# Optimization experiments

Measured on AMD Instinct MI355X. Metric: run time of the kernel, lower is better.

The kernel has to match this reference:

```python
import jax, jax.numpy as jnp
import numpy as np

B, T, E = 4, 2048, 512      # batch, seq_len, embedding_dim
H, D = 8, 64                # n_heads, head_size


def setup_inputs() -> dict:
    key = jax.random.key(0)
    ks = jax.random.split(key, 8)
    rn = lambda k, sh, sc=1.0: jax.random.normal(k, sh, dtype=jnp.float32) * sc
    return {
        "x": rn(ks[0], (B, T, E)),
        "k": rn(ks[1], (B, T, E)),
        "q": rn(ks[2], (B, T, E)),
        "v": rn(ks[3], (B, T, E)),
        # per-head Q/K/V projection weights, stacked: [H, D, E] (bias=False as in nanoGPT-style heads)
        "Wq": rn(ks[4], (H, D, E), E ** -0.5),
        "Wk": rn(ks[5], (H, D, E), E ** -0.5),
        "Wv": rn(ks[6], (H, D, E), E ** -0.5),
        # output projection Linear(H*D -> E)
        "Wo": rn(ks[7], (E, H * D), (H * D) ** -0.5),
        "bo": jnp.zeros((E,), jnp.float32),
    }


def reference(x, k, q, v, Wq, Wk, Wv, Wo, bo):
    # batched equivalent of the per-head Python loop: one einsum per Q/K/V
    qh = jnp.einsum('bte,hde->bhtd', q, Wq)   # [B,H,T,D]
    kh = jnp.einsum('bse,hde->bhsd', k, Wk)
    vh = jnp.einsum('bse,hde->bhsd', v, Wv)
    scores = jnp.einsum('bhtd,bhsd->bhts', qh, kh) * (D ** -0.5)
    Tq = x.shape[1]
    causal = jnp.tril(jnp.ones((Tq, Tq), dtype=bool))  # masked=True: tril mask
    scores = jnp.where(causal, scores, -jnp.inf)
    wei = jax.nn.softmax(scores, axis=-1)              # dropout=0.0 -> identity
    out = jnp.einsum('bhts,bhsd->bhtd', wei, vh)       # [B,H,T,D]
    out = out.transpose(0, 2, 1, 3).reshape(x.shape[0], Tq, H * D)  # concat heads
    return out @ Wo.T + bo                              # final projection
```

## Files before the change

### kernel.cpp

```cpp
#include <hip/hip_runtime.h>
#include <hip/hip_bf16.h>
#include <cstdint>
#include <cstddef>

#define Bb 4
#define Tt 2048
#define Ee 512
#define Hh 8
#define Dd 64
#define HD 512
#define BT 8192

typedef __bf16 bf16x8 __attribute__((ext_vector_type(8)));
typedef __bf16 bf16x4 __attribute__((ext_vector_type(4)));
typedef short s16x4 __attribute__((ext_vector_type(4)));
typedef float f32x4 __attribute__((ext_vector_type(4)));

__device__ __forceinline__ f32x4 mfma16(bf16x8 a, bf16x8 b, f32x4 c) {
  return __builtin_amdgcn_mfma_f32_16x16x32_bf16(a, b, c, 0, 0, 0);
}

__device__ __forceinline__ s16x4 as_s16x4(bf16x4 v) {
  union { bf16x4 b; s16x4 s; } u; u.b = v; return u.s;
}

__device__ __forceinline__ f32x4 mfma16k16(bf16x4 a, bf16x4 b, f32x4 c) {
#if defined(__HIP_DEVICE_COMPILE__)
  return __builtin_amdgcn_mfma_f32_16x16x16bf16_1k(as_s16x4(a), as_s16x4(b), c, 0, 0, 0);
#else
  (void)a; (void)b;
  return c;
#endif
}

typedef __attribute__((address_space(3))) uint32_t lds_u32_t;
typedef const __attribute__((address_space(1))) uint32_t glb_u32_t;
__device__ __forceinline__ void gload16(const void* g, void* l) {
  __builtin_amdgcn_global_load_lds((glb_u32_t*)g, (lds_u32_t*)l, 16, 0, 0);
}

__global__ void cvt_w_kernel(const float* __restrict__ wq, const float* __restrict__ wk,
                             const float* __restrict__ wv, const float* __restrict__ wo,
                             __bf16* __restrict__ dst) {
  int id = blockIdx.x * 256 + threadIdx.x;
  int r = id & 127;
  int lgg = (id >> 7) & 3;
  int p = (id >> 9) & 15;
  int cb = (id >> 13) & 3;
  int m = id >> 15;
  const float* src = (m == 0) ? wq : (m == 1) ? wk : (m == 2) ? wv : wo;
  const float* s = src + (size_t)(cb * 128 + r) * 512 + p * 32 + lgg * 8;
  float4 f0 = *(const float4*)s;
  float4 f1 = *(const float4*)(s + 4);
  bf16x8 o;
  o[0] = (__bf16)f0.x; o[1] = (__bf16)f0.y; o[2] = (__bf16)f0.z; o[3] = (__bf16)f0.w;
  o[4] = (__bf16)f1.x; o[5] = (__bf16)f1.y; o[6] = (__bf16)f1.z; o[7] = (__bf16)f1.w;
  *(bf16x8*)(dst + (size_t)m * 262144 + cb * 65536 + p * 4096 + lgg * 1024 + r * 8) = o;
}

__global__ __launch_bounds__(256)
void gemm_qkv_kernel(const float* __restrict__ Aq, const float* __restrict__ Ak,
                     const float* __restrict__ Av, const __bf16* __restrict__ Wall,
                     __bf16* __restrict__ qh, __bf16* __restrict__ kh, __bf16* __restrict__ vt) {
  const int id = blockIdx.x;
  const int xcd = id & 7, s = id >> 3;
  const int bx = s & 3;
  const int pair = xcd + 8 * (s >> 2);
  const int by = pair & 63;
  const int pz = pair >> 6;

  const float* A = (pz == 0) ? Aq : (pz == 1) ? Ak : Av;
  const char* Bw = (const char*)(Wall + (size_t)pz * 262144 + (size_t)bx * 65536);
  const int row0 = by * 128;
  const int col0 = bx * 128;

  __shared__ __align__(16) __bf16 As[128 * 32];
  __shared__ __align__(16) __bf16 Bs[128 * 32];
  char* As8 = (char*)As;
  char* Bs8 = (char*)Bs;

  const int tid = threadIdx.x;
  const int l = tid & 63, w = tid >> 6;
  const int ln = l & 15, lg = l >> 4;
  const int wr = (w >> 1) * 64, wc = (w & 1) * 64;

  const int sr = tid >> 1;
  const int sce = (tid & 1) * 16;
  const int sbyte = sr * 64 + sce * 2;
  const int swz = (sr & 7) << 4;

  f32x4 acc[4][4] = {};

  const float* agbase = A + (size_t)(row0 + sr) * Ee + sce;
  float4 a0 = *(const float4*)(agbase);
  float4 a1 = *(const float4*)(agbase + 4);
  float4 a2 = *(const float4*)(agbase + 8);
  float4 a3 = *(const float4*)(agbase + 12);

  for (int ktp = 0; ktp < 16; ktp++) {
    bf16x8 c0, c1;
    c0[0] = (__bf16)a0.x; c0[1] = (__bf16)a0.y; c0[2] = (__bf16)a0.z; c0[3] = (__bf16)a0.w;
    c0[4] = (__bf16)a1.x; c0[5] = (__bf16)a1.y; c0[6] = (__bf16)a1.z; c0[7] = (__bf16)a1.w;
    c1[0] = (__bf16)a2.x; c1[1] = (__bf16)a2.y; c1[2] = (__bf16)a2.z; c1[3] = (__bf16)a2.w;
    c1[4] = (__bf16)a3.x; c1[5] = (__bf16)a3.y; c1[6] = (__bf16)a3.z; c1[7] = (__bf16)a3.w;
    __syncthreads();
    {
      const char* pb = Bw + ktp * 8192;
      gload16(pb + w * 2048 + l * 16, Bs8 + w * 2048);
      gload16(pb + w * 2048 + 1024 + l * 16, Bs8 + w * 2048 + 1024);
    }
    *(bf16x8*)(As8 + ((sbyte) ^ swz)) = c0;
    *(bf16x8*)(As8 + ((sbyte + 16) ^ swz)) = c1;
    if (ktp < 15) {
      const float* ag = agbase + (ktp + 1) * 32;
      a0 = *(const float4*)(ag);
      a1 = *(const float4*)(ag + 4);
      a2 = *(const float4*)(ag + 8);
      a3 = *(const float4*)(ag + 12);
    }
    __builtin_amdgcn_sched_barrier(0);
    __syncthreads();
    bf16x8 af[4], bfr[4];
#pragma unroll
    for (int mi = 0; mi < 4; mi++) {
      int r = wr + mi * 16 + ln;
      af[mi] = *(const bf16x8*)(As8 + ((r * 64 + lg * 16) ^ ((r & 7) << 4)));
    }
#pragma unroll
    for (int ni = 0; ni < 4; ni++) {
      int rr = wc + ni * 16 + ln;
      bfr[ni] = *(const bf16x8*)(Bs8 + lg * 2048 + rr * 16);
    }
#pragma unroll
    for (int mi = 0; mi < 4; mi++)
#pragma unroll
      for (int ni = 0; ni < 4; ni++)
        acc[mi][ni] = mfma16(af[mi], bfr[ni], acc[mi][ni]);
  }

  const float sc = (pz == 0) ? 0.18033688011112042f : 1.0f;
#pragma unroll
  for (int mi = 0; mi < 4; mi++) {
    const int rowb = row0 + wr + mi * 16 + lg * 4;
    const int bb = rowb >> 11;
    const int t0 = rowb & (Tt - 1);
#pragma unroll
    for (int ni = 0; ni < 4; ni++) {
      const int colb = col0 + wc + ni * 16 + ln;
      const int hh = colb >> 6;
      const int dd = colb & 63;
      if (pz == 2) {
        bf16x4 pk;
#pragma unroll
        for (int r = 0; r < 4; r++) pk[r] = (__bf16)acc[mi][ni][r];
        *(bf16x4*)(vt + (size_t)(bb * Hh + hh) * 131072 +
                   (t0 >> 6) * 4096 + ((t0 & 63) >> 2) * 256 + dd * 4) = pk;
      } else {
        __bf16* dstp = (pz == 0 ? qh : kh) + ((size_t)(bb * Hh + hh) * Tt + t0) * Dd + dd;
#pragma unroll
        for (int r = 0; r < 4; r++) dstp[(size_t)r * Dd] = (__bf16)(acc[mi][ni][r] * sc);
      }
    }
  }
}

__global__ __launch_bounds__(512)
void attn1_kernel(const __bf16* __restrict__ qh, const __bf16* __restrict__ kh,
                  const __bf16* __restrict__ vt, __bf16* __restrict__ opart,
                  float* __restrict__ lpart) {
  const int j = blockIdx.x;
  const int xcd = j & 7, slot = j >> 3;
  const int ck = slot & 1;
  const int pp = (slot >> 1) & 15;
  const int bhi = slot >> 5;
  const int bh = xcd + 8 * bhi;

  __shared__ __align__(16) char Kb[2][8192];
  __shared__ __align__(16) char Vb[2][8192];

  const int tid = threadIdx.x;
  const int l = tid & 63, w = tid >> 6;
  const int ln = l & 15, lg = l >> 4;
  const int grp = w >> 2, wg = w & 3;

  const char* Kg = (const char*)(kh + (size_t)bh * Tt * Dd);
  const char* Vg = (const char*)(vt + (size_t)bh * 131072);
  const __bf16* Q = qh + (size_t)bh * Tt * Dd;

  const int rsub = l >> 3;
  const int csw = ((l & 7) ^ rsub) * 16;
  const int cb = ck * 32 + bh;

  const int qt = grp ? (31 - pp) : pp;
  const int n = qt + 1;
  const int nmax = 32 - pp;
  const int qr = qt * 64 + wg * 16;

  bf16x4 ones;
#pragma unroll
  for (int r = 0; r < 4; r++) ones[r] = (__bf16)1.0f;

  f32x4 oacc[4] = {};
  f32x4 lsum = {};

  {
    const char* kt = Kg + (size_t)ck * 8192;
    const char* vtile = Vg + (size_t)ck * 8192;
    gload16(kt + (w * 8 + rsub) * 128 + csw, (char*)Kb[0] + w * 1024);
    gload16(vtile + w * 1024 + l * 16, (char*)Vb[0] + w * 1024);
  }

  bf16x8 qf[2];
#pragma unroll
  for (int kk = 0; kk < 2; kk++)
    qf[kk] = *(const bf16x8*)(Q + (size_t)(qr + ln) * Dd + kk * 32 + lg * 8);

  for (int st = ck; st < nmax; st += 2) {
    const int cur = ((st - ck) >> 1) & 1;
    asm volatile("s_waitcnt vmcnt(0)" ::: "memory");
    __builtin_amdgcn_s_barrier();
    __builtin_amdgcn_sched_barrier(0);
    if (st + 2 < nmax) {
      const char* kt = Kg + (size_t)(st + 2) * 8192;
      const char* vtile = Vg + (size_t)(st + 2) * 8192;
      gload16(kt + (w * 8 + rsub) * 128 + csw, (char*)Kb[cur ^ 1] + w * 1024);
      gload16(vtile + w * 1024 + l * 16, (char*)Vb[cur ^ 1] + w * 1024);
    }
    if (st < n) {
      const char* KB = Kb[cur];
      const char* VB = Vb[cur];
      const int s0 = st * 64;

      f32x4 sacc[4] = {};
      __builtin_amdgcn_s_setprio(1);
#pragma unroll
      for (int kk = 0; kk < 2; kk++) {
#pragma unroll
        for (int ni = 0; ni < 4; ni++) {
          bf16x8 kf = *(const bf16x8*)(KB + (ni * 16 + ln) * 128 + (((kk * 4 + lg) ^ (ln & 7)) * 16));
          sacc[ni] = mfma16(kf, qf[kk], sacc[ni]);
        }
      }
      __builtin_amdgcn_s_setprio(0);

      if (st == qt) {
#pragma unroll
        for (int ni = 0; ni < 4; ni++)
#pragma unroll
          for (int r = 0; r < 4; r++)
            if ((s0 + ni * 16 + lg * 4 + r) > (qr + ln)) sacc[ni][r] = -1e30f;
      }

      bf16x4 pk[4];
#pragma unroll
      for (int ni = 0; ni < 4; ni++)
#pragma unroll
        for (int r = 0; r < 4; r++)
          pk[ni][r] = (__bf16)__builtin_amdgcn_exp2f(sacc[ni][r]);

      __builtin_amdgcn_s_setprio(1);
#pragma unroll
      for (int nd = 0; nd < 4; nd++) {
        const char* vrow = VB + (nd * 16 + ln) * 8 + lg * 512;
#pragma unroll
        for (int ni = 0; ni < 4; ni++) {
          bf16x4 vfr = *(const bf16x4*)(vrow + ni * 2048);
          oacc[nd] = mfma16k16(vfr, pk[ni], oacc[nd]);
        }
      }
#pragma unroll
      for (int ni = 0; ni < 4; ni++)
        lsum = mfma16k16(ones, pk[ni], lsum);
      __builtin_amdgcn_s_setprio(0);
    }
  }

#pragma unroll
  for (int nd = 0; nd < 4; nd++) {
    bf16x4 ov;
#pragma unroll
    for (int r = 0; r < 4; r++) ov[r] = (__bf16)oacc[nd][r];
    *(bf16x4*)(opart + ((size_t)cb * Tt + qr + ln) * 64 + nd * 16 + lg * 4) = ov;
  }
  if (l < 16) {
    lpart[(size_t)cb * Tt + qr + l] = lsum[0];
  }
}

__global__ __launch_bounds__(256)
void gemm_out_kernel(const __bf16* __restrict__ opart, const float* __restrict__ lpart,
                     const __bf16* __restrict__ Wall, const float* __restrict__ bo,
                     float* __restrict__ out) {
  const int id = blockIdx.x;
  const int xcd = id & 7, s = id >> 3;
  const int bx = s & 3;
  const int by = xcd + 8 * (s >> 2);

  const int row0 = by * 64;
  const int col0 = bx * 128;
  const char* Bw = (const char*)(Wall + (size_t)3 * 262144 + (size_t)bx * 65536);

  __shared__ __align__(16) __bf16 As[64 * 32];
  __shared__ __align__(16) __bf16 Bs[128 * 32];
  char* As8 = (char*)As;
  char* Bs8 = (char*)Bs;

  const int tid = threadIdx.x;
  const int l = tid & 63, w = tid >> 6;
  const int ln = l & 15, lg = l >> 4;
  const int wr = (w >> 1) * 32, wc = (w & 1) * 64;

  const int sr = tid >> 2;
  const int q = tid & 3;
  const int abyte = sr * 64 + q * 16;
  const int aswz = (sr & 7) << 4;

  const int srow = row0 + sr;
  const int b = srow >> 11, t = srow & (Tt - 1);

  f32x4 acc[2][4] = {};

  int c = q * 8;
  int h = c >> 6;
  size_t i0 = ((size_t)(b * Hh + h) * Tt + t) * 64 + (c & 63);
  bf16x8 v0 = *(const bf16x8*)(opart + i0);
  bf16x8 v1 = *(const bf16x8*)(opart + i0 + (size_t)32 * Tt * 64);
  float l0 = lpart[(size_t)(b * Hh + h) * Tt + t];
  float l1 = lpart[(size_t)(32 + b * Hh + h) * Tt + t];

  for (int ktp = 0; ktp < 16; ktp++) {
    float rden = 1.0f / (l0 + l1);
    bf16x8 c0;
#pragma unroll
    for (int e = 0; e < 8; e++)
      c0[e] = (__bf16)(((float)v0[e] + (float)v1[e]) * rden);
    __syncthreads();
    {
      const char* pb = Bw + ktp * 8192;
      gload16(pb + w * 2048 + l * 16, Bs8 + w * 2048);
      gload16(pb + w * 2048 + 1024 + l * 16, Bs8 + w * 2048 + 1024);
    }
    *(bf16x8*)(As8 + (abyte ^ aswz)) = c0;
    if (ktp < 15) {
      c = (ktp + 1) * 32 + q * 8;
      h = c >> 6;
      i0 = ((size_t)(b * Hh + h) * Tt + t) * 64 + (c & 63);
      v0 = *(const bf16x8*)(opart + i0);
      v1 = *(const bf16x8*)(opart + i0 + (size_t)32 * Tt * 64);
      l0 = lpart[(size_t)(b * Hh + h) * Tt + t];
      l1 = lpart[(size_t)(32 + b * Hh + h) * Tt + t];
    }
    __builtin_amdgcn_sched_barrier(0);
    __syncthreads();
    bf16x8 af[2], bfr[4];
#pragma unroll
    for (int mi = 0; mi < 2; mi++) {
      int r = wr + mi * 16 + ln;
      af[mi] = *(const bf16x8*)(As8 + ((r * 64 + lg * 16) ^ ((r & 7) << 4)));
    }
#pragma unroll
    for (int ni = 0; ni < 4; ni++) {
      int rr = wc + ni * 16 + ln;
      bfr[ni] = *(const bf16x8*)(Bs8 + lg * 2048 + rr * 16);
    }
#pragma unroll
    for (int mi = 0; mi < 2; mi++)
#pragma unroll
      for (int ni = 0; ni < 4; ni++)
        acc[mi][ni] = mfma16(af[mi], bfr[ni], acc[mi][ni]);
  }

#pragma unroll
  for (int mi = 0; mi < 2; mi++) {
    const int rowb = row0 + wr + mi * 16 + lg * 4;
#pragma unroll
    for (int ni = 0; ni < 4; ni++) {
      const int col = col0 + wc + ni * 16 + ln;
      const float bias = bo[col];
#pragma unroll
      for (int r = 0; r < 4; r++)
        out[(size_t)(rowb + r) * Ee + col] = acc[mi][ni][r] + bias;
    }
  }
}

extern "C" void kernel_launch(void* const* d_in, const int* in_sizes, int n_in,
                              void* d_out, int out_size, void* d_ws, size_t ws_size,
                              hipStream_t stream) {
  (void)in_sizes; (void)n_in; (void)out_size; (void)ws_size;
  const float* kin = (const float*)d_in[1];
  const float* qin = (const float*)d_in[2];
  const float* vin = (const float*)d_in[3];
  const float* Wq = (const float*)d_in[4];
  const float* Wk = (const float*)d_in[5];
  const float* Wv = (const float*)d_in[6];
  const float* Wo = (const float*)d_in[7];
  const float* bo = (const float*)d_in[8];
  float* out = (float*)d_out;

  __bf16* wall = (__bf16*)d_ws;
  __bf16* qh = wall + (size_t)1048576;
  __bf16* kh = qh + (size_t)4194304;
  __bf16* vt = kh + (size_t)4194304;
  __bf16* opart = vt + (size_t)4194304;
  float* lpart = (float*)(opart + (size_t)8388608);

  cvt_w_kernel<<<dim3(512), dim3(256), 0, stream>>>(Wq, Wk, Wv, Wo, wall);
  gemm_qkv_kernel<<<dim3(768), dim3(256), 0, stream>>>(qin, kin, vin, wall, qh, kh, vt);
  attn1_kernel<<<dim3(1024), dim3(512), 0, stream>>>(qh, kh, vt, opart, lpart);
  gemm_out_kernel<<<dim3(512), dim3(256), 0, stream>>>(opart, lpart, wall, bo, out);
}
```

Baseline: 81.87 us.

## Pre-convert QKV activations to bf16 and double-buffer the QKV GEMM loads

Adds a separate kernel that converts the q/k/v fp32 activations into a bf16 tiled layout in workspace. The QKV GEMM then streams both A and B tiles with direct global-to-LDS loads into double-buffered shared memory, and drops the in-register fp32 conversion and one barrier per k-step. The cost is an extra kernel launch plus a full fp32 read and bf16 write/read round trip of the activations. The opart buffer is moved to alias the new activation buffer to save workspace.

```diff
diff --git a/kernel.cpp b/kernel.cpp
--- a/kernel.cpp
+++ b/kernel.cpp
@@ -58,9 +58,32 @@
   *(bf16x8*)(dst + (size_t)m * 262144 + cb * 65536 + p * 4096 + lgg * 1024 + r * 8) = o;
 }
 
+__global__ void cvt_a_kernel(const float* __restrict__ aq, const float* __restrict__ ak,
+                             const float* __restrict__ av, __bf16* __restrict__ dst) {
+  const int blk = blockIdx.x;
+  const int p = blk & 15;
+  const int y = (blk >> 4) & 63;
+  const int m = blk >> 10;
+  const int tid = threadIdx.x;
+  const int r = tid >> 1, half = tid & 1;
+  const float* src = (m == 0) ? aq : (m == 1) ? ak : av;
+  const float* s = src + (size_t)(y * 128 + r) * 512 + p * 32 + half * 16;
+  float4 f0 = *(const float4*)s;
+  float4 f1 = *(const float4*)(s + 4);
+  float4 f2 = *(const float4*)(s + 8);
+  float4 f3 = *(const float4*)(s + 12);
+  bf16x8 o0, o1;
+  o0[0] = (__bf16)f0.x; o0[1] = (__bf16)f0.y; o0[2] = (__bf16)f0.z; o0[3] = (__bf16)f0.w;
+  o0[4] = (__bf16)f1.x; o0[5] = (__bf16)f1.y; o0[6] = (__bf16)f1.z; o0[7] = (__bf16)f1.w;
+  o1[0] = (__bf16)f2.x; o1[1] = (__bf16)f2.y; o1[2] = (__bf16)f2.z; o1[3] = (__bf16)f2.w;
+  o1[4] = (__bf16)f3.x; o1[5] = (__bf16)f3.y; o1[6] = (__bf16)f3.z; o1[7] = (__bf16)f3.w;
+  __bf16* d = dst + (size_t)m * 4194304 + y * 65536 + p * 4096 + (half * 2) * 1024 + r * 8;
+  *(bf16x8*)(d) = o0;
+  *(bf16x8*)(d + 1024) = o1;
+}
+
 __global__ __launch_bounds__(256)
-void gemm_qkv_kernel(const float* __restrict__ Aq, const float* __restrict__ Ak,
-                     const float* __restrict__ Av, const __bf16* __restrict__ Wall,
+void gemm_qkv_kernel(const __bf16* __restrict__ Aall, const __bf16* __restrict__ Wall,
                      __bf16* __restrict__ qh, __bf16* __restrict__ kh, __bf16* __restrict__ vt) {
   const int id = blockIdx.x;
   const int xcd = id & 7, s = id >> 3;
@@ -69,13 +92,13 @@
   const int by = pair & 63;
   const int pz = pair >> 6;
 
-  const float* A = (pz == 0) ? Aq : (pz == 1) ? Ak : Av;
+  const char* Aw = (const char*)(Aall + (size_t)pz * 4194304 + (size_t)by * 65536);
   const char* Bw = (const char*)(Wall + (size_t)pz * 262144 + (size_t)bx * 65536);
   const int row0 = by * 128;
   const int col0 = bx * 128;
 
-  __shared__ __align__(16) __bf16 As[128 * 32];
-  __shared__ __align__(16) __bf16 Bs[128 * 32];
+  __shared__ __align__(16) __bf16 As[2][4096];
+  __shared__ __align__(16) __bf16 Bs[2][4096];
   char* As8 = (char*)As;
   char* Bs8 = (char*)Bs;
 
@@ -84,58 +107,43 @@
   const int ln = l & 15, lg = l >> 4;
   const int wr = (w >> 1) * 64, wc = (w & 1) * 64;
 
-  const int sr = tid >> 1;
-  const int sce = (tid & 1) * 16;
-  const int sbyte = sr * 64 + sce * 2;
-  const int swz = (sr & 7) << 4;
-
   f32x4 acc[4][4] = {};
 
-  const float* agbase = A + (size_t)(row0 + sr) * Ee + sce;
-  float4 a0 = *(const float4*)(agbase);
-  float4 a1 = *(const float4*)(agbase + 4);
-  float4 a2 = *(const float4*)(agbase + 8);
-  float4 a3 = *(const float4*)(agbase + 12);
-
+  gload16(Aw + w * 2048 + l * 16, As8 + w * 2048);
+  gload16(Aw + w * 2048 + 1024 + l * 16, As8 + w * 2048 + 1024);
+  gload16(Bw + w * 2048 + l * 16, Bs8 + w * 2048);
+  gload16(Bw + w * 2048 + 1024 + l * 16, Bs8 + w * 2048 + 1024);
+
+  int cur = 0;
   for (int ktp = 0; ktp < 16; ktp++) {
-    bf16x8 c0, c1;
-    c0[0] = (__bf16)a0.x; c0[1] = (__bf16)a0.y; c0[2] = (__bf16)a0.z; c0[3] = (__bf16)a0.w;
-    c0[4] = (__bf16)a1.x; c0[5] = (__bf16)a1.y; c0[6] = (__bf16)a1.z; c0[7] = (__bf16)a1.w;
-    c1[0] = (__bf16)a2.x; c1[1] = (__bf16)a2.y; c1[2] = (__bf16)a2.z; c1[3] = (__bf16)a2.w;
-    c1[4] = (__bf16)a3.x; c1[5] = (__bf16)a3.y; c1[6] = (__bf16)a3.z; c1[7] = (__bf16)a3.w;
     __syncthreads();
-    {
-      const char* pb = Bw + ktp * 8192;
-      gload16(pb + w * 2048 + l * 16, Bs8 + w * 2048);
-      gload16(pb + w * 2048 + 1024 + l * 16, Bs8 + w * 2048 + 1024);
-    }
-    *(bf16x8*)(As8 + ((sbyte) ^ swz)) = c0;
-    *(bf16x8*)(As8 + ((sbyte + 16) ^ swz)) = c1;
     if (ktp < 15) {
-      const float* ag = agbase + (ktp + 1) * 32;
-      a0 = *(const float4*)(ag);
-      a1 = *(const float4*)(ag + 4);
-      a2 = *(const float4*)(ag + 8);
-      a3 = *(const float4*)(ag + 12);
-    }
-    __builtin_amdgcn_sched_barrier(0);
-    __syncthreads();
+      const char* pa = Aw + (ktp + 1) * 8192;
+      const char* pb = Bw + (ktp + 1) * 8192;
+      char* da = As8 + (cur ^ 1) * 8192;
+      char* db = Bs8 + (cur ^ 1) * 8192;
+      gload16(pa + w * 2048 + l * 16, da + w * 2048);
+      gload16(pa + w * 2048 + 1024 + l * 16, da + w * 2048 + 1024);
+      gload16(pb + w * 2048 + l * 16, db + w * 2048);
+      gload16(pb + w * 2048 + 1024 + l * 16, db + w * 2048 + 1024);
+    }
     bf16x8 af[4], bfr[4];
 #pragma unroll
     for (int mi = 0; mi < 4; mi++) {
       int r = wr + mi * 16 + ln;
-      af[mi] = *(const bf16x8*)(As8 + ((r * 64 + lg * 16) ^ ((r & 7) << 4)));
+      af[mi] = *(const bf16x8*)(As8 + cur * 8192 + lg * 2048 + r * 16);
     }
 #pragma unroll
     for (int ni = 0; ni < 4; ni++) {
       int rr = wc + ni * 16 + ln;
-      bfr[ni] = *(const bf16x8*)(Bs8 + lg * 2048 + rr * 16);
+      bfr[ni] = *(const bf16x8*)(Bs8 + cur * 8192 + lg * 2048 + rr * 16);
     }
 #pragma unroll
     for (int mi = 0; mi < 4; mi++)
 #pragma unroll
       for (int ni = 0; ni < 4; ni++)
         acc[mi][ni] = mfma16(af[mi], bfr[ni], acc[mi][ni]);
+    cur ^= 1;
   }
 
   const float sc = (pz == 0) ? 0.18033688011112042f : 1.0f;
@@ -399,14 +407,16 @@
   float* out = (float*)d_out;
 
   __bf16* wall = (__bf16*)d_ws;
-  __bf16* qh = wall + (size_t)1048576;
+  __bf16* abuf = wall + (size_t)1048576;
+  __bf16* qh = abuf + (size_t)12582912;
   __bf16* kh = qh + (size_t)4194304;
   __bf16* vt = kh + (size_t)4194304;
-  __bf16* opart = vt + (size_t)4194304;
+  __bf16* opart = abuf;
   float* lpart = (float*)(opart + (size_t)8388608);
 
   cvt_w_kernel<<<dim3(512), dim3(256), 0, stream>>>(Wq, Wk, Wv, Wo, wall);
-  gemm_qkv_kernel<<<dim3(768), dim3(256), 0, stream>>>(qin, kin, vin, wall, qh, kh, vt);
+  cvt_a_kernel<<<dim3(3072), dim3(256), 0, stream>>>(qin, kin, vin, abuf);
+  gemm_qkv_kernel<<<dim3(768), dim3(256), 0, stream>>>(abuf, wall, qh, kh, vt);
   attn1_kernel<<<dim3(1024), dim3(512), 0, stream>>>(qh, kh, vt, opart, lpart);
   gemm_out_kernel<<<dim3(512), dim3(256), 0, stream>>>(opart, lpart, wall, bo, out);
 }
```

New measurement: 89.26 us. +9.0%, slower.
